# Kernel optimization log

Hardware: AMD Instinct MI355X
Metric: run time of the kernel (lower is better)

## Reference

```python
import jax, jax.numpy as jnp
import numpy as np


def setup_inputs() -> dict:
    key = jax.random.key(0)
    ks = jax.random.split(key, 6)
    B, T, D, H = 2, 2048, 1024, 16
    dk = D // H
    s = 0.02
    return {
        "x": jax.random.normal(ks[0], (B, T, D), dtype=jnp.float32),
        "Wq": jax.random.normal(ks[1], (H, dk, dk), dtype=jnp.float32) * s,
        "Wk": jax.random.normal(ks[2], (H, dk, dk), dtype=jnp.float32) * s,
        "Wv": jax.random.normal(ks[3], (H, dk, dk), dtype=jnp.float32) * s,
        "Wp": jax.random.normal(ks[4], (D, D), dtype=jnp.float32) * s,
        "bp": jnp.zeros((D,), dtype=jnp.float32),
    }


def reference(x, Wq, Wk, Wv, Wp, bp):
    B, T, D = x.shape
    H, dk, _ = Wq.shape
    # split into heads: [B, H, T, dk]
    xh = x.reshape(B, T, H, dk).transpose(0, 2, 1, 3)
    # per-head torch Linear (y = x @ W^T), all heads at once
    q = jnp.einsum('bhtd,hkd->bhtk', xh, Wq)
    k = jnp.einsum('bhtd,hkd->bhtk', xh, Wk)
    v = jnp.einsum('bhtd,hkd->bhtk', xh, Wv)
    scale = 1.0 / jnp.sqrt(jnp.float32(dk))  # original divides by sqrt(C) with C == d_k
    scores = jnp.einsum('bhqd,bhkd->bhqk', q, k) * scale
    causal = jnp.tril(jnp.ones((T, T), dtype=bool))
    scores = jnp.where(causal[None, None], scores, -jnp.inf)
    attn = jax.nn.softmax(scores, axis=-1)
    out = jnp.einsum('bhqk,bhkd->bhqd', attn, v)  # [B,H,T,dk]
    out = out.transpose(0, 2, 1, 3).reshape(B, T, D)  # concat heads
    return out @ Wp.T + bp
```

## Files before the change

### kernel.cpp

```cpp
#include <hip/hip_runtime.h>
#include <math.h>

#define B_ 2
#define T_ 2048
#define D_ 1024
#define H_ 16
#define DK 64
#define BH_ (B_*H_)

typedef __attribute__((ext_vector_type(8))) short short8;
typedef __attribute__((ext_vector_type(4))) short bf16x4;
typedef __attribute__((ext_vector_type(4))) float fragC;

#if defined(__HIP_DEVICE_COMPILE__)
#define MFMA16(A,B,C) __builtin_amdgcn_mfma_f32_16x16x16bf16_1k((A),(B),(C),0,0,0)
#else
#define MFMA16(A,B,C) (C)
#endif
#define MFMA32(A,B,C) __builtin_amdgcn_mfma_f32_16x16x32_bf16((A),(B),(C),0,0,0)

__device__ __forceinline__ unsigned short f2bf(float x) {
    union { float f; unsigned u; } c; c.f = x;
    unsigned r = c.u + 0x7fff + ((c.u >> 16) & 1);
    return (unsigned short)(r >> 16);
}

__device__ __forceinline__ unsigned pack2bf(float a, float b) {
    return (unsigned)f2bf(a) | ((unsigned)f2bf(b) << 16);
}

__device__ __forceinline__ unsigned permpack(float a, float b) {
    union { float f; unsigned u; } ca, cb; ca.f = a; cb.f = b;
    return __builtin_amdgcn_perm(cb.u, ca.u, 0x07060302);
}

__device__ __forceinline__ short8 packbf8(float4 a, float4 b) {
    union { short8 v; unsigned u[4]; } r;
    r.u[0] = pack2bf(a.x, a.y); r.u[1] = pack2bf(a.z, a.w);
    r.u[2] = pack2bf(b.x, b.y); r.u[3] = pack2bf(b.z, b.w);
    return r.v;
}

__device__ __forceinline__ void gload_lds16(const void* g, void* l) {
    __builtin_amdgcn_global_load_lds(
        (const __attribute__((address_space(1))) unsigned int*)g,
        (__attribute__((address_space(3))) unsigned int*)l, 16, 0, 0);
}

__global__ __launch_bounds__(256) void cvt_kernel(
    const float* __restrict__ Wp,
    const float* __restrict__ Wq, const float* __restrict__ Wk,
    const float* __restrict__ Wv,
    unsigned short* __restrict__ Wb, unsigned short* __restrict__ wqkvb)
{
    const int gid = blockIdx.x * 256 + threadIdx.x;
    const float* src; unsigned short* dst;
    if (gid < 131072) { src = Wp + (size_t)gid * 8; dst = Wb + (size_t)gid * 8; }
    else              { int e = gid - 131072;
                        int mat = e >> 13, rem = e & 8191;
                        int h = rem >> 9, od = rem & 511;
                        const float* ws = (mat == 0) ? Wq : (mat == 1) ? Wk : Wv;
                        src = ws + ((size_t)(h << 9) + od) * 8;
                        dst = wqkvb + ((size_t)h*1536 + mat*512 + od) * 8; }
    float4 a = *(const float4*)src;
    float4 b = *(const float4*)(src + 4);
    *(uint4*)dst = make_uint4(pack2bf(a.x, a.y), pack2bf(a.z, a.w),
                              pack2bf(b.x, b.y), pack2bf(b.z, b.w));
}

__global__ __launch_bounds__(256) void qkv_kernel(
    const float* __restrict__ x,
    const unsigned short* __restrict__ wqkvb,
    unsigned short* __restrict__ q, unsigned short* __restrict__ k,
    unsigned short* __restrict__ vt)
{
    __shared__ unsigned short Wl[3*64*64];

    const int bh = blockIdx.x;
    const int b  = bh >> 4, h = bh & 15;
    const int t0 = blockIdx.y * 128;
    const int tid = threadIdx.x;
    const int wave = tid >> 6, lane = tid & 63;
    const int n = lane & 15, quad = lane >> 4;

    {
        const unsigned short* wsrc = wqkvb + (size_t)h * 12288;
        #pragma unroll
        for (int j = 0; j < 6; ++j) {
            const int off = (wave*6 + j) * 512 + lane*8;
            gload_lds16(wsrc + off, &Wl[off]);
        }
    }

    const int tw = t0 + wave*32;
    short8 xf[2][2];
    #pragma unroll
    for (int rt = 0; rt < 2; ++rt) {
        const float* xr = &x[((size_t)b*T_ + tw + rt*16 + n)*D_ + h*DK];
        float4 a0 = *(const float4*)&xr[quad*8];
        float4 a1 = *(const float4*)&xr[quad*8 + 4];
        xf[rt][0] = packbf8(a0, a1);
        float4 b0 = *(const float4*)&xr[32 + quad*8];
        float4 b1 = *(const float4*)&xr[32 + quad*8 + 4];
        xf[rt][1] = packbf8(b0, b1);
    }
    __syncthreads();

    const float qsc = 0.125f * 1.44269504088896340736f;
    const int tb0 = blockIdx.y*8 + wave*2;
    #pragma unroll
    for (int mat = 0; mat < 3; ++mat) {
        const int wbase = mat * 4096;
        #pragma unroll
        for (int ct = 0; ct < 4; ++ct) {
            short8 wf0 = *(const short8*)&Wl[wbase + (ct*16 + n)*64 + quad*8];
            short8 wf1 = *(const short8*)&Wl[wbase + (ct*16 + n)*64 + 32 + quad*8];
            #pragma unroll
            for (int rt = 0; rt < 2; ++rt) {
                fragC z = {0.f,0.f,0.f,0.f};
                if (mat < 2) {
                    z = MFMA32(wf0, xf[rt][0], z);
                    z = MFMA32(wf1, xf[rt][1], z);
                    if (mat == 0) {
                        z[0] *= qsc; z[1] *= qsc; z[2] *= qsc; z[3] *= qsc;
                    }
                    unsigned short* dstg = (mat == 0) ? q : k;
                    unsigned short* dp = &dstg[((size_t)bh*128 + tb0 + rt)*1024
                                               + (ct*2 + (quad>>1))*128 + n*8 + (quad&1)*4];
                    *(uint2*)dp = make_uint2(pack2bf(z[0], z[1]), pack2bf(z[2], z[3]));
                } else {
                    z = MFMA32(xf[rt][0], wf0, z);
                    z = MFMA32(xf[rt][1], wf1, z);
                    const int key0 = tw + rt*16;
                    const int ktv = key0 >> 6, ctv = (key0 >> 4) & 3;
                    unsigned short* dp = &vt[(size_t)bh*131072 + ktv*4096
                                             + ct*1024 + ctv*256 + quad*64 + n*4];
                    *(uint2*)dp = make_uint2(pack2bf(z[0], z[1]), pack2bf(z[2], z[3]));
                }
            }
        }
    }
}

__global__ __launch_bounds__(256, 4) void attn_kernel(
    const unsigned short* __restrict__ q, const unsigned short* __restrict__ k,
    const unsigned short* __restrict__ vt, unsigned short* __restrict__ aout)
{
    __shared__ unsigned short Ks[2][4096];
    __shared__ unsigned short Vs[2][4096];

    const int id = blockIdx.x;
    int qt, bh;
    if (id < 512) { bh = id >> 4;         qt = 31 - (id & 15); }
    else          { bh = (id - 512) >> 4; qt = (id - 512) & 15; }

    const int b   = bh >> 4, h = bh & 15;
    const int tid = threadIdx.x;
    const int wave = tid >> 6, lane = tid & 63;
    const int n = lane & 15, quad = lane >> 4;
    const int q0 = qt*64 + wave*16;

    const unsigned short* qb = &q[((size_t)bh*128 + qt*4 + wave)*1024 + n*8];
    short8 qf0 = *(const short8*)&qb[quad*128];
    short8 qf1 = *(const short8*)&qb[(4 + quad)*128];

    fragC o[4];
    #pragma unroll
    for (int dt = 0; dt < 4; ++dt) o[dt] = (fragC){0.f,0.f,0.f,0.f};
    fragC l4 = {0.f,0.f,0.f,0.f};

    bf16x4 ones4;
    #pragma unroll
    for (int j = 0; j < 4; ++j) ones4[j] = (short)0x3F80;

    const unsigned short* kg = &k[(size_t)bh*131072];
    const unsigned short* vg = &vt[(size_t)bh*131072];

    const int nt = qt + 1;
    gload_lds16(kg + tid*8,        &Ks[0][tid*8]);
    gload_lds16(kg + 2048 + tid*8, &Ks[0][2048 + tid*8]);
    gload_lds16(vg + tid*8,        &Vs[0][tid*8]);
    gload_lds16(vg + 2048 + tid*8, &Vs[0][2048 + tid*8]);

    for (int kt = 0; kt < nt; ++kt) {
        __syncthreads();
        if (kt + 1 < nt) {
            const int nb = (kt + 1) & 1;
            const unsigned short* kgn = kg + (size_t)(kt+1)*4096;
            const unsigned short* vgn = vg + (size_t)(kt+1)*4096;
            gload_lds16(kgn + tid*8,        &Ks[nb][tid*8]);
            gload_lds16(kgn + 2048 + tid*8, &Ks[nb][2048 + tid*8]);
            gload_lds16(vgn + tid*8,        &Vs[nb][tid*8]);
            gload_lds16(vgn + 2048 + tid*8, &Vs[nb][2048 + tid*8]);
        }
        const unsigned short* Kb = Ks[kt & 1];
        const unsigned short* Vb = Vs[kt & 1];
        const bool diag = (kt == qt);

        bf16x4 pp[4];
        #pragma unroll
        for (int ct = 0; ct < 4; ++ct) {
            short8 kf0 = *(const short8*)&Kb[ct*1024 + quad*128 + n*8];
            short8 kf1 = *(const short8*)&Kb[ct*1024 + 512 + quad*128 + n*8];
            fragC c = {0.f,0.f,0.f,0.f};
            c = MFMA32(kf0, qf0, c);
            c = MFMA32(kf1, qf1, c);
            float p0 = exp2f(c[0]), p1 = exp2f(c[1]);
            float p2 = exp2f(c[2]), p3 = exp2f(c[3]);
            if (diag) {
                const int lim = (wave*16 + n) - (ct*16 + quad*4);
                if (0 > lim) p0 = 0.f;
                if (1 > lim) p1 = 0.f;
                if (2 > lim) p2 = 0.f;
                if (3 > lim) p3 = 0.f;
            }
            union { bf16x4 v; unsigned u[2]; } pk;
            pk.u[0] = permpack(p0, p1);
            pk.u[1] = permpack(p2, p3);
            pp[ct] = pk.v;
        }
        #pragma unroll
        for (int ct = 0; ct < 4; ++ct)
            l4 = MFMA16(ones4, pp[ct], l4);
        #pragma unroll
        for (int dt = 0; dt < 4; ++dt) {
            #pragma unroll
            for (int ct = 0; ct < 4; ++ct) {
                bf16x4 vf = *(const bf16x4*)&Vb[dt*1024 + ct*256 + quad*64 + n*4];
                o[dt] = MFMA16(vf, pp[ct], o[dt]);
            }
        }
    }

    const float inv = 1.0f / l4[0];
    unsigned short* dp = &aout[((size_t)b*T_ + q0 + n)*D_ + h*DK + quad*4];
    #pragma unroll
    for (int dt = 0; dt < 4; ++dt) {
        *(uint2*)(dp + dt*16) =
            make_uint2(pack2bf(o[dt][0]*inv, o[dt][1]*inv),
                       pack2bf(o[dt][2]*inv, o[dt][3]*inv));
    }
}

__global__ __launch_bounds__(256) void proj_kernel(
    const unsigned short* __restrict__ A, const unsigned short* __restrict__ Wb,
    const float* __restrict__ bp, float* __restrict__ out)
{
    __shared__ unsigned short As[128*64];
    __shared__ unsigned short Bs[128*64];

    const int m0 = blockIdx.x * 128, n0 = blockIdx.y * 128;
    const int tid = threadIdx.x;
    const int wave = tid >> 6, lane = tid & 63;
    const int wm = wave & 1, wn = wave >> 1;
    const int n = lane & 15, quad = lane >> 4;

    const int srow = wave*32 + (lane >> 3);
    const int scol = (lane & 7) * 8;
    const unsigned short* ag = &A [(size_t)(m0 + srow)*1024 + scol];
    const unsigned short* bg = &Wb[(size_t)(n0 + srow)*1024 + scol];
    unsigned short* al = &As[(size_t)srow*64 + scol];
    unsigned short* bl = &Bs[(size_t)srow*64 + scol];

    fragC acc[4][4];
    #pragma unroll
    for (int i = 0; i < 4; ++i)
        #pragma unroll
        for (int j = 0; j < 4; ++j) acc[i][j] = (fragC){0.f,0.f,0.f,0.f};

    for (int kt = 0; kt < 16; ++kt) {
        __syncthreads();
        #pragma unroll
        for (int i = 0; i < 4; ++i) {
            gload_lds16(ag + (size_t)i*8*1024 + kt*64, al + i*8*64);
            gload_lds16(bg + (size_t)i*8*1024 + kt*64, bl + i*8*64);
        }
        __syncthreads();

        #pragma unroll
        for (int kk = 0; kk < 2; ++kk) {
            short8 af[4], bf[4];
            #pragma unroll
            for (int i = 0; i < 4; ++i)
                af[i] = *(const short8*)&As[(wm*64 + i*16 + n)*64 + kk*32 + quad*8];
            #pragma unroll
            for (int j = 0; j < 4; ++j)
                bf[j] = *(const short8*)&Bs[(wn*64 + j*16 + n)*64 + kk*32 + quad*8];
            #pragma unroll
            for (int i = 0; i < 4; ++i)
                #pragma unroll
                for (int j = 0; j < 4; ++j)
                    acc[i][j] = MFMA32(af[i], bf[j], acc[i][j]);
        }
    }

    #pragma unroll
    for (int i = 0; i < 4; ++i) {
        #pragma unroll
        for (int r = 0; r < 4; ++r) {
            const int m = m0 + wm*64 + i*16 + quad*4 + r;
            #pragma unroll
            for (int j = 0; j < 4; ++j) {
                const int col = n0 + wn*64 + j*16 + n;
                out[(size_t)m*1024 + col] = acc[i][j][r] + bp[col];
            }
        }
    }
}

extern "C" void kernel_launch(void* const* d_in, const int* in_sizes, int n_in,
                              void* d_out, int out_size, void* d_ws, size_t ws_size,
                              hipStream_t stream)
{
    const float* x  = (const float*)d_in[0];
    const float* Wq = (const float*)d_in[1];
    const float* Wk = (const float*)d_in[2];
    const float* Wv = (const float*)d_in[3];
    const float* Wp = (const float*)d_in[4];
    const float* bp = (const float*)d_in[5];
    float* out = (float*)d_out;

    const size_t per = (size_t)BH_ * T_ * DK;
    unsigned short* qws   = (unsigned short*)d_ws;
    unsigned short* kws   = qws + per;
    unsigned short* vtws  = kws + per;
    unsigned short* aws   = vtws + per;
    unsigned short* wbws  = aws + per;
    unsigned short* wqkvb = wbws + 1024*1024;

    cvt_kernel<<<dim3(608), 256, 0, stream>>>(Wp, Wq, Wk, Wv, wbws, wqkvb);
    qkv_kernel<<<dim3(BH_, T_/128), 256, 0, stream>>>(x, wqkvb, qws, kws, vtws);
    attn_kernel<<<dim3(1024), 256, 0, stream>>>(qws, kws, vtws, aws);
    proj_kernel<<<dim3(32, 8), 256, 0, stream>>>(aws, wbws, bp, out);
}
```

Before: 149.3 us.

## Rebalance work: paired causal q-tiles per attention block, smaller QKV and proj tiles

The attention kernel now gives each block two query tiles (e and 31-e), so every block does the same total causal work. The grid shrinks to 512 blocks that run the two passes in sequence. The QKV kernel halves its per-block token tile, and the projection GEMM uses 64x128 tiles, doubling the block count for better CU occupancy. In exchange, each projection block reuses less data, and the attention passes run serially within a block with an extra pipeline restart between them.

```diff
diff --git a/kernel.cpp b/kernel.cpp
--- a/kernel.cpp
+++ b/kernel.cpp
@@ -78,7 +78,7 @@
 
     const int bh = blockIdx.x;
     const int b  = bh >> 4, h = bh & 15;
-    const int t0 = blockIdx.y * 128;
+    const int t0 = blockIdx.y * 64;
     const int tid = threadIdx.x;
     const int wave = tid >> 6, lane = tid & 63;
     const int n = lane & 15, quad = lane >> 4;
@@ -92,22 +92,22 @@
         }
     }
 
-    const int tw = t0 + wave*32;
-    short8 xf[2][2];
-    #pragma unroll
-    for (int rt = 0; rt < 2; ++rt) {
-        const float* xr = &x[((size_t)b*T_ + tw + rt*16 + n)*D_ + h*DK];
+    const int tw = t0 + wave*16;
+    short8 xf[2];
+    {
+        const float* xr = &x[((size_t)b*T_ + tw + n)*D_ + h*DK];
         float4 a0 = *(const float4*)&xr[quad*8];
         float4 a1 = *(const float4*)&xr[quad*8 + 4];
-        xf[rt][0] = packbf8(a0, a1);
+        xf[0] = packbf8(a0, a1);
         float4 b0 = *(const float4*)&xr[32 + quad*8];
         float4 b1 = *(const float4*)&xr[32 + quad*8 + 4];
-        xf[rt][1] = packbf8(b0, b1);
+        xf[1] = packbf8(b0, b1);
     }
     __syncthreads();
 
     const float qsc = 0.125f * 1.44269504088896340736f;
-    const int tb0 = blockIdx.y*8 + wave*2;
+    const int tb0 = blockIdx.y*4 + wave;
+    const int ktv = tw >> 6, ctv = (tw >> 4) & 3;
     #pragma unroll
     for (int mat = 0; mat < 3; ++mat) {
         const int wbase = mat * 4096;
@@ -115,28 +115,23 @@
         for (int ct = 0; ct < 4; ++ct) {
             short8 wf0 = *(const short8*)&Wl[wbase + (ct*16 + n)*64 + quad*8];
             short8 wf1 = *(const short8*)&Wl[wbase + (ct*16 + n)*64 + 32 + quad*8];
-            #pragma unroll
-            for (int rt = 0; rt < 2; ++rt) {
-                fragC z = {0.f,0.f,0.f,0.f};
-                if (mat < 2) {
-                    z = MFMA32(wf0, xf[rt][0], z);
-                    z = MFMA32(wf1, xf[rt][1], z);
-                    if (mat == 0) {
-                        z[0] *= qsc; z[1] *= qsc; z[2] *= qsc; z[3] *= qsc;
-                    }
-                    unsigned short* dstg = (mat == 0) ? q : k;
-                    unsigned short* dp = &dstg[((size_t)bh*128 + tb0 + rt)*1024
-                                               + (ct*2 + (quad>>1))*128 + n*8 + (quad&1)*4];
-                    *(uint2*)dp = make_uint2(pack2bf(z[0], z[1]), pack2bf(z[2], z[3]));
-                } else {
-                    z = MFMA32(xf[rt][0], wf0, z);
-                    z = MFMA32(xf[rt][1], wf1, z);
-                    const int key0 = tw + rt*16;
-                    const int ktv = key0 >> 6, ctv = (key0 >> 4) & 3;
-                    unsigned short* dp = &vt[(size_t)bh*131072 + ktv*4096
-                                             + ct*1024 + ctv*256 + quad*64 + n*4];
-                    *(uint2*)dp = make_uint2(pack2bf(z[0], z[1]), pack2bf(z[2], z[3]));
+            fragC z = {0.f,0.f,0.f,0.f};
+            if (mat < 2) {
+                z = MFMA32(wf0, xf[0], z);
+                z = MFMA32(wf1, xf[1], z);
+                if (mat == 0) {
+                    z[0] *= qsc; z[1] *= qsc; z[2] *= qsc; z[3] *= qsc;
                 }
+                unsigned short* dstg = (mat == 0) ? q : k;
+                unsigned short* dp = &dstg[((size_t)bh*128 + tb0)*1024
+                                           + (ct*2 + (quad>>1))*128 + n*8 + (quad&1)*4];
+                *(uint2*)dp = make_uint2(pack2bf(z[0], z[1]), pack2bf(z[2], z[3]));
+            } else {
+                z = MFMA32(xf[0], wf0, z);
+                z = MFMA32(xf[1], wf1, z);
+                unsigned short* dp = &vt[(size_t)bh*131072 + ktv*4096
+                                         + ct*1024 + ctv*256 + quad*64 + n*4];
+                *(uint2*)dp = make_uint2(pack2bf(z[0], z[1]), pack2bf(z[2], z[3]));
             }
         }
     }
@@ -150,24 +145,13 @@
     __shared__ unsigned short Vs[2][4096];
 
     const int id = blockIdx.x;
-    int qt, bh;
-    if (id < 512) { bh = id >> 4;         qt = 31 - (id & 15); }
-    else          { bh = (id - 512) >> 4; qt = (id - 512) & 15; }
+    const int bh = id >> 4;
+    const int e  = id & 15;
 
     const int b   = bh >> 4, h = bh & 15;
     const int tid = threadIdx.x;
     const int wave = tid >> 6, lane = tid & 63;
     const int n = lane & 15, quad = lane >> 4;
-    const int q0 = qt*64 + wave*16;
-
-    const unsigned short* qb = &q[((size_t)bh*128 + qt*4 + wave)*1024 + n*8];
-    short8 qf0 = *(const short8*)&qb[quad*128];
-    short8 qf1 = *(const short8*)&qb[(4 + quad)*128];
-
-    fragC o[4];
-    #pragma unroll
-    for (int dt = 0; dt < 4; ++dt) o[dt] = (fragC){0.f,0.f,0.f,0.f};
-    fragC l4 = {0.f,0.f,0.f,0.f};
 
     bf16x4 ones4;
     #pragma unroll
@@ -176,69 +160,85 @@
     const unsigned short* kg = &k[(size_t)bh*131072];
     const unsigned short* vg = &vt[(size_t)bh*131072];
 
-    const int nt = qt + 1;
-    gload_lds16(kg + tid*8,        &Ks[0][tid*8]);
-    gload_lds16(kg + 2048 + tid*8, &Ks[0][2048 + tid*8]);
-    gload_lds16(vg + tid*8,        &Vs[0][tid*8]);
-    gload_lds16(vg + 2048 + tid*8, &Vs[0][2048 + tid*8]);
-
-    for (int kt = 0; kt < nt; ++kt) {
-        __syncthreads();
-        if (kt + 1 < nt) {
-            const int nb = (kt + 1) & 1;
-            const unsigned short* kgn = kg + (size_t)(kt+1)*4096;
-            const unsigned short* vgn = vg + (size_t)(kt+1)*4096;
-            gload_lds16(kgn + tid*8,        &Ks[nb][tid*8]);
-            gload_lds16(kgn + 2048 + tid*8, &Ks[nb][2048 + tid*8]);
-            gload_lds16(vgn + tid*8,        &Vs[nb][tid*8]);
-            gload_lds16(vgn + 2048 + tid*8, &Vs[nb][2048 + tid*8]);
-        }
-        const unsigned short* Kb = Ks[kt & 1];
-        const unsigned short* Vb = Vs[kt & 1];
-        const bool diag = (kt == qt);
-
-        bf16x4 pp[4];
-        #pragma unroll
-        for (int ct = 0; ct < 4; ++ct) {
-            short8 kf0 = *(const short8*)&Kb[ct*1024 + quad*128 + n*8];
-            short8 kf1 = *(const short8*)&Kb[ct*1024 + 512 + quad*128 + n*8];
-            fragC c = {0.f,0.f,0.f,0.f};
-            c = MFMA32(kf0, qf0, c);
-            c = MFMA32(kf1, qf1, c);
-            float p0 = exp2f(c[0]), p1 = exp2f(c[1]);
-            float p2 = exp2f(c[2]), p3 = exp2f(c[3]);
-            if (diag) {
-                const int lim = (wave*16 + n) - (ct*16 + quad*4);
-                if (0 > lim) p0 = 0.f;
-                if (1 > lim) p1 = 0.f;
-                if (2 > lim) p2 = 0.f;
-                if (3 > lim) p3 = 0.f;
-            }
-            union { bf16x4 v; unsigned u[2]; } pk;
-            pk.u[0] = permpack(p0, p1);
-            pk.u[1] = permpack(p2, p3);
-            pp[ct] = pk.v;
-        }
-        #pragma unroll
-        for (int ct = 0; ct < 4; ++ct)
-            l4 = MFMA16(ones4, pp[ct], l4);
+    #pragma unroll
+    for (int pass = 0; pass < 2; ++pass) {
+        const int qt = pass ? (31 - e) : e;
+        const int q0 = qt*64 + wave*16;
+        const int nt = qt + 1;
+
+        const unsigned short* qb = &q[((size_t)bh*128 + qt*4 + wave)*1024 + n*8];
+        short8 qf0 = *(const short8*)&qb[quad*128];
+        short8 qf1 = *(const short8*)&qb[(4 + quad)*128];
+
+        fragC o[4];
+        #pragma unroll
+        for (int dt = 0; dt < 4; ++dt) o[dt] = (fragC){0.f,0.f,0.f,0.f};
+        fragC l4 = {0.f,0.f,0.f,0.f};
+
+        if (pass) __syncthreads();
+        gload_lds16(kg + tid*8,        &Ks[0][tid*8]);
+        gload_lds16(kg + 2048 + tid*8, &Ks[0][2048 + tid*8]);
+        gload_lds16(vg + tid*8,        &Vs[0][tid*8]);
+        gload_lds16(vg + 2048 + tid*8, &Vs[0][2048 + tid*8]);
+
+        for (int kt = 0; kt < nt; ++kt) {
+            __syncthreads();
+            if (kt + 1 < nt) {
+                const int nb = (kt + 1) & 1;
+                const unsigned short* kgn = kg + (size_t)(kt+1)*4096;
+                const unsigned short* vgn = vg + (size_t)(kt+1)*4096;
+                gload_lds16(kgn + tid*8,        &Ks[nb][tid*8]);
+                gload_lds16(kgn + 2048 + tid*8, &Ks[nb][2048 + tid*8]);
+                gload_lds16(vgn + tid*8,        &Vs[nb][tid*8]);
+                gload_lds16(vgn + 2048 + tid*8, &Vs[nb][2048 + tid*8]);
+            }
+            const unsigned short* Kb = Ks[kt & 1];
+            const unsigned short* Vb = Vs[kt & 1];
+            const bool diag = (kt == qt);
+
+            bf16x4 pp[4];
+            #pragma unroll
+            for (int ct = 0; ct < 4; ++ct) {
+                short8 kf0 = *(const short8*)&Kb[ct*1024 + quad*128 + n*8];
+                short8 kf1 = *(const short8*)&Kb[ct*1024 + 512 + quad*128 + n*8];
+                fragC c = {0.f,0.f,0.f,0.f};
+                c = MFMA32(kf0, qf0, c);
+                c = MFMA32(kf1, qf1, c);
+                float p0 = exp2f(c[0]), p1 = exp2f(c[1]);
+                float p2 = exp2f(c[2]), p3 = exp2f(c[3]);
+                if (diag) {
+                    const int lim = (wave*16 + n) - (ct*16 + quad*4);
+                    if (0 > lim) p0 = 0.f;
+                    if (1 > lim) p1 = 0.f;
+                    if (2 > lim) p2 = 0.f;
+                    if (3 > lim) p3 = 0.f;
+                }
+                union { bf16x4 v; unsigned u[2]; } pk;
+                pk.u[0] = permpack(p0, p1);
+                pk.u[1] = permpack(p2, p3);
+                pp[ct] = pk.v;
+            }
+            #pragma unroll
+            for (int ct = 0; ct < 4; ++ct)
+                l4 = MFMA16(ones4, pp[ct], l4);
+            #pragma unroll
+            for (int dt = 0; dt < 4; ++dt) {
+                #pragma unroll
+                for (int ct = 0; ct < 4; ++ct) {
+                    bf16x4 vf = *(const bf16x4*)&Vb[dt*1024 + ct*256 + quad*64 + n*4];
+                    o[dt] = MFMA16(vf, pp[ct], o[dt]);
+                }
+            }
+        }
+
+        const float inv = 1.0f / l4[0];
+        unsigned short* dp = &aout[((size_t)b*T_ + q0 + n)*D_ + h*DK + quad*4];
         #pragma unroll
         for (int dt = 0; dt < 4; ++dt) {
-            #pragma unroll
-            for (int ct = 0; ct < 4; ++ct) {
-                bf16x4 vf = *(const bf16x4*)&Vb[dt*1024 + ct*256 + quad*64 + n*4];
-                o[dt] = MFMA16(vf, pp[ct], o[dt]);
-            }
-        }
-    }
-
-    const float inv = 1.0f / l4[0];
-    unsigned short* dp = &aout[((size_t)b*T_ + q0 + n)*D_ + h*DK + quad*4];
-    #pragma unroll
-    for (int dt = 0; dt < 4; ++dt) {
-        *(uint2*)(dp + dt*16) =
-            make_uint2(pack2bf(o[dt][0]*inv, o[dt][1]*inv),
-                       pack2bf(o[dt][2]*inv, o[dt][3]*inv));
+            *(uint2*)(dp + dt*16) =
+                make_uint2(pack2bf(o[dt][0]*inv, o[dt][1]*inv),
+                           pack2bf(o[dt][2]*inv, o[dt][3]*inv));
+        }
     }
 }
 
@@ -246,50 +246,51 @@
     const unsigned short* __restrict__ A, const unsigned short* __restrict__ Wb,
     const float* __restrict__ bp, float* __restrict__ out)
 {
-    __shared__ unsigned short As[128*64];
+    __shared__ unsigned short As[64*64];
     __shared__ unsigned short Bs[128*64];
 
-    const int m0 = blockIdx.x * 128, n0 = blockIdx.y * 128;
+    const int m0 = blockIdx.x * 64, n0 = blockIdx.y * 128;
     const int tid = threadIdx.x;
     const int wave = tid >> 6, lane = tid & 63;
-    const int wm = wave & 1, wn = wave >> 1;
     const int n = lane & 15, quad = lane >> 4;
 
-    const int srow = wave*32 + (lane >> 3);
-    const int scol = (lane & 7) * 8;
-    const unsigned short* ag = &A [(size_t)(m0 + srow)*1024 + scol];
-    const unsigned short* bg = &Wb[(size_t)(n0 + srow)*1024 + scol];
-    unsigned short* al = &As[(size_t)srow*64 + scol];
-    unsigned short* bl = &Bs[(size_t)srow*64 + scol];
-
-    fragC acc[4][4];
+    const int srowB = wave*32 + (lane >> 3);
+    const int srowA = wave*16 + (lane >> 3);
+    const int scol  = (lane & 7) * 8;
+    const unsigned short* ag = &A [(size_t)(m0 + srowA)*1024 + scol];
+    const unsigned short* bg = &Wb[(size_t)(n0 + srowB)*1024 + scol];
+    unsigned short* al = &As[(size_t)srowA*64 + scol];
+    unsigned short* bl = &Bs[(size_t)srowB*64 + scol];
+
+    fragC acc[4][2];
     #pragma unroll
     for (int i = 0; i < 4; ++i)
         #pragma unroll
-        for (int j = 0; j < 4; ++j) acc[i][j] = (fragC){0.f,0.f,0.f,0.f};
+        for (int j = 0; j < 2; ++j) acc[i][j] = (fragC){0.f,0.f,0.f,0.f};
 
     for (int kt = 0; kt < 16; ++kt) {
         __syncthreads();
         #pragma unroll
-        for (int i = 0; i < 4; ++i) {
+        for (int i = 0; i < 2; ++i)
             gload_lds16(ag + (size_t)i*8*1024 + kt*64, al + i*8*64);
+        #pragma unroll
+        for (int i = 0; i < 4; ++i)
             gload_lds16(bg + (size_t)i*8*1024 + kt*64, bl + i*8*64);
-        }
         __syncthreads();
 
         #pragma unroll
         for (int kk = 0; kk < 2; ++kk) {
-            short8 af[4], bf[4];
+            short8 af[4], bf[2];
             #pragma unroll
             for (int i = 0; i < 4; ++i)
-                af[i] = *(const short8*)&As[(wm*64 + i*16 + n)*64 + kk*32 + quad*8];
-            #pragma unroll
-            for (int j = 0; j < 4; ++j)
-                bf[j] = *(const short8*)&Bs[(wn*64 + j*16 + n)*64 + kk*32 + quad*8];
+                af[i] = *(const short8*)&As[(i*16 + n)*64 + kk*32 + quad*8];
+            #pragma unroll
+            for (int j = 0; j < 2; ++j)
+                bf[j] = *(const short8*)&Bs[(wave*32 + j*16 + n)*64 + kk*32 + quad*8];
             #pragma unroll
             for (int i = 0; i < 4; ++i)
                 #pragma unroll
-                for (int j = 0; j < 4; ++j)
+                for (int j = 0; j < 2; ++j)
                     acc[i][j] = MFMA32(af[i], bf[j], acc[i][j]);
         }
     }
@@ -298,10 +299,10 @@
     for (int i = 0; i < 4; ++i) {
         #pragma unroll
         for (int r = 0; r < 4; ++r) {
-            const int m = m0 + wm*64 + i*16 + quad*4 + r;
-            #pragma unroll
-            for (int j = 0; j < 4; ++j) {
-                const int col = n0 + wn*64 + j*16 + n;
+            const int m = m0 + i*16 + quad*4 + r;
+            #pragma unroll
+            for (int j = 0; j < 2; ++j) {
+                const int col = n0 + wave*32 + j*16 + n;
                 out[(size_t)m*1024 + col] = acc[i][j][r] + bp[col];
             }
         }
@@ -329,7 +330,7 @@
     unsigned short* wqkvb = wbws + 1024*1024;
 
     cvt_kernel<<<dim3(608), 256, 0, stream>>>(Wp, Wq, Wk, Wv, wbws, wqkvb);
-    qkv_kernel<<<dim3(BH_, T_/128), 256, 0, stream>>>(x, wqkvb, qws, kws, vtws);
-    attn_kernel<<<dim3(1024), 256, 0, stream>>>(qws, kws, vtws, aws);
-    proj_kernel<<<dim3(32, 8), 256, 0, stream>>>(aws, wbws, bp, out);
-}
+    qkv_kernel<<<dim3(BH_, T_/64), 256, 0, stream>>>(x, wqkvb, qws, kws, vtws);
+    attn_kernel<<<dim3(512), 256, 0, stream>>>(qws, kws, vtws, aws);
+    proj_kernel<<<dim3(64, 8), 256, 0, stream>>>(aws, wbws, bp, out);
+}
```

Result: no change. 151.6 us (+1.5%).
